# Performance work log

Measured on AMD Instinct MI355X. Metric: run time of the kernel, lower is better.

Reference implementation:

```python
import jax, jax.numpy as jnp
import numpy as np

D_MODEL = 1024
NUM_HEADS = 16
D_HEAD = D_MODEL // NUM_HEADS
MAX_SEQ_LEN = 4096
ROPE_THETA = 10000.0


def _rope_tables():
    freqs = 1.0 / (ROPE_THETA ** (jnp.arange(0, D_HEAD, 2, dtype=jnp.float32) / D_HEAD))
    pos = jnp.arange(MAX_SEQ_LEN, dtype=jnp.float32)
    ang = jnp.outer(pos, freqs)  # [max_seq, d_head/2]
    return jnp.cos(ang), jnp.sin(ang)


def apply_rope(x, token_positions, cos_tab, sin_tab):
    # x: [..., seq, d_head], token_positions: [batch, seq]
    cos = cos_tab[token_positions]  # [batch, seq, d_head/2]
    sin = sin_tab[token_positions]
    x_even = x[..., 0::2]
    x_odd = x[..., 1::2]
    e = x_even * cos - x_odd * sin
    o = x_even * sin + x_odd * cos
    # interleave back
    out = jnp.stack([e, o], axis=-1).reshape(x.shape)
    return out


def setup_inputs() -> dict:
    key = jax.random.key(0)
    k_x, k_q, k_k, k_v, k_o = jax.random.split(key, 5)
    B, S = 1, 4096
    x = jax.random.normal(k_x, (B, S, D_MODEL), dtype=jnp.float32)
    token_positions = jnp.broadcast_to(jnp.arange(S, dtype=jnp.int32)[None, :], (B, S))
    # trunc_normal init approximated by normal clipped to [-2, 2]
    def tn(k):
        return jnp.clip(jax.random.normal(k, (D_MODEL, D_MODEL), dtype=jnp.float32), -2.0, 2.0)
    return {
        "x": x,
        "token_positions": token_positions,
        "w_q": tn(k_q),
        "w_k": tn(k_k),
        "w_v": tn(k_v),
        "w_o": tn(k_o),
    }


def reference(x, token_positions, w_q, w_k, w_v, w_o):
    B, S, _ = x.shape
    cos_tab, sin_tab = _rope_tables()

    # Linear: y = x @ W^T  (weight is [out, in])
    Q = jnp.einsum('bsd,ed->bse', x, w_q)
    K = jnp.einsum('bsd,ed->bse', x, w_k)
    V = jnp.einsum('bsd,ed->bse', x, w_v)

    # [B, H, S, d_head]
    Q = Q.reshape(B, S, NUM_HEADS, D_HEAD).transpose(0, 2, 1, 3)
    K = K.reshape(B, S, NUM_HEADS, D_HEAD).transpose(0, 2, 1, 3)
    V = V.reshape(B, S, NUM_HEADS, D_HEAD).transpose(0, 2, 1, 3)

    # RoPE on Q, K (broadcast cos/sin over head dim)
    cos = cos_tab[token_positions][:, None]  # [B,1,S,d_head/2]
    sin = sin_tab[token_positions][:, None]
    def rope(t):
        e, o = t[..., 0::2], t[..., 1::2]
        return jnp.stack([e * cos - o * sin, e * sin + o * cos], axis=-1).reshape(t.shape)
    Q = rope(Q)
    K = rope(K)

    scale = 1.0 / jnp.sqrt(jnp.float32(D_HEAD))
    scores = jnp.einsum('bhqd,bhkd->bhqk', Q, K) * scale
    causal = jnp.tril(jnp.ones((S, S), dtype=bool))
    scores = jnp.where(causal, scores, -jnp.inf)
    probs = jax.nn.softmax(scores, axis=-1)
    attn = jnp.einsum('bhqk,bhkd->bhqd', probs, V)

    attn = attn.transpose(0, 2, 1, 3).reshape(B, S, D_MODEL)
    out = jnp.einsum('bsd,ed->bse', attn, w_o)
    return out
```

## Files before the change

kernel.cpp:

```cpp
#include <hip/hip_runtime.h>
#include <hip/hip_bf16.h>
#include <math.h>

#define S_LEN 4096
#define DMODEL 1024
#define NHEADS 16
#define DHEAD 64

typedef unsigned short u16;
typedef short bf16x8 __attribute__((ext_vector_type(8)));
typedef float f32x4 __attribute__((ext_vector_type(4)));
typedef u16 u16x4 __attribute__((ext_vector_type(4)));
typedef u16 u16x8 __attribute__((ext_vector_type(8)));
typedef unsigned uint4v __attribute__((ext_vector_type(4)));
typedef unsigned uint2v __attribute__((ext_vector_type(2)));

__device__ __forceinline__ u16 f2bf(float f) {
    unsigned u = __builtin_bit_cast(unsigned, f);
    u = (u + 0x7FFFu + ((u >> 16) & 1u)) >> 16;
    return (u16)u;
}
__device__ __forceinline__ float bf2f(u16 b) {
    return __builtin_bit_cast(float, ((unsigned)b) << 16);
}
__device__ __forceinline__ unsigned pack2bf(float lo, float hi) {
    __hip_bfloat162 c = __float22bfloat162_rn(make_float2(lo, hi));
    unsigned u;
    __builtin_memcpy(&u, &c, 4);
    return u;
}

__device__ __forceinline__ void gload16(const void* g, void* l) {
    __builtin_amdgcn_global_load_lds((const __attribute__((address_space(1))) void*)g,
                                     (__attribute__((address_space(3))) void*)l, 16, 0, 0);
}

__global__ void rope_table_kernel(float* __restrict__ cost, float* __restrict__ sint) {
    int tid = blockIdx.x * blockDim.x + threadIdx.x;
    int i = tid & 31;
    int pos = tid >> 5;
    double e = (double)(2 * i) / 64.0;
    float t32 = (float)pow(10000.0, e);
    float freq = 1.0f / t32;
    float ang = (float)pos * freq;
    cost[tid] = (float)cos((double)ang);
    sint[tid] = (float)sin((double)ang);
}

__global__ void split_kernel(const float* __restrict__ in, u16* __restrict__ hi,
                             u16* __restrict__ lo, int n4) {
    int i = blockIdx.x * blockDim.x + threadIdx.x;
    if (i >= n4) return;
    float4 v = ((const float4*)in)[i];
    float f[4] = {v.x, v.y, v.z, v.w};
    u16x4 h, l;
#pragma unroll
    for (int j = 0; j < 4; j++) {
        h[j] = f2bf(f[j]);
        l[j] = f2bf(f[j] - bf2f(h[j]));
    }
    ((u16x4*)hi)[i] = h;
    if (lo) ((u16x4*)lo)[i] = l;
}

__global__ __launch_bounds__(256) void gemm_qkv_kernel(
        const u16* __restrict__ xh, const u16* __restrict__ xl,
        const u16* __restrict__ wh3, const u16* __restrict__ wl3,
        const int* __restrict__ tp,
        const float* __restrict__ cost, const float* __restrict__ sint,
        u16* __restrict__ q2, u16* __restrict__ k2, u16* __restrict__ vtb) {
    __shared__ u16 sAH[2][128 * 32], sAL[2][128 * 32], sBH[2][128 * 32], sBL[2][128 * 32];
    const int z = blockIdx.z;
    const bool full = (z != 2);
    const u16* BH = wh3 + (size_t)z * 1048576;
    const u16* BL = wl3 + (size_t)z * 1048576;
    const int m0 = blockIdx.y * 128, n0 = blockIdx.x * 128;

    const int tid = threadIdx.x;
    const int lane = tid & 63, wid = tid >> 6;
    const int wr = wid >> 1, wc = wid & 1;
    const int l15 = lane & 15, lhi = lane >> 4;

    f32x4 acc[4][4];
#pragma unroll
    for (int i = 0; i < 4; i++)
#pragma unroll
        for (int j = 0; j < 4; j++) acc[i][j] = (f32x4){0.f, 0.f, 0.f, 0.f};

    auto stageT = [&](int kt, int b) {
#pragma unroll
        for (int i = 0; i < 2; i++) {
            const int rbase = wid * 32 + i * 16;
            const int row = rbase + (lane >> 2);
            const size_t aoff = (size_t)(m0 + row) * 1024 + kt + (lane & 3) * 8;
            const size_t boff = (size_t)(n0 + row) * 1024 + kt + (lane & 3) * 8;
            gload16(xh + aoff, sAH[b] + rbase * 32);
            gload16(BH + boff, sBH[b] + rbase * 32);
            if (full) {
                gload16(xl + aoff, sAL[b] + rbase * 32);
                gload16(BL + boff, sBL[b] + rbase * 32);
            }
        }
    };

    stageT(0, 0);
    __syncthreads();

    int buf = 0;
    for (int kt = 0; kt < 1024; kt += 32, buf ^= 1) {
        if (kt + 32 < 1024) stageT(kt + 32, buf ^ 1);
        bf16x8 ah[4], al[4], bh[4], bl[4];
#pragma unroll
        for (int m = 0; m < 4; m++) {
            int row = wr * 64 + m * 16 + l15;
            ah[m] = *(const bf16x8*)(sAH[buf] + row * 32 + 8 * lhi);
            if (full) al[m] = *(const bf16x8*)(sAL[buf] + row * 32 + 8 * lhi);
        }
#pragma unroll
        for (int n = 0; n < 4; n++) {
            int row = wc * 64 + n * 16 + l15;
            bh[n] = *(const bf16x8*)(sBH[buf] + row * 32 + 8 * lhi);
            if (full) bl[n] = *(const bf16x8*)(sBL[buf] + row * 32 + 8 * lhi);
        }
#pragma unroll
        for (int m = 0; m < 4; m++)
#pragma unroll
            for (int n = 0; n < 4; n++) {
                if (full) {
                    acc[m][n] = __builtin_amdgcn_mfma_f32_16x16x32_bf16(al[m], bh[n], acc[m][n], 0, 0, 0);
                    acc[m][n] = __builtin_amdgcn_mfma_f32_16x16x32_bf16(ah[m], bl[n], acc[m][n], 0, 0, 0);
                }
                acc[m][n] = __builtin_amdgcn_mfma_f32_16x16x32_bf16(ah[m], bh[n], acc[m][n], 0, 0, 0);
            }
        __syncthreads();
    }

    if (z == 2) {
#pragma unroll
        for (int m = 0; m < 4; m++)
#pragma unroll
            for (int n = 0; n < 4; n++)
#pragma unroll
                for (int j = 0; j < 4; j++) {
                    int srow = m0 + wr * 64 + m * 16 + lhi * 4 + j;
                    int eg = n0 + wc * 64 + n * 16 + l15;
                    vtb[(size_t)eg * S_LEN + srow] = f2bf(acc[m][n][j]);
                }
        return;
    }

    u16* outp = (z == 0) ? q2 : k2;
    const float qscale = (z == 0) ? 0.125f : 1.0f;
    const int head = (n0 + wc * 64) >> 6;
#pragma unroll
    for (int m = 0; m < 4; m++)
#pragma unroll
        for (int n = 0; n < 4; n++) {
            const int dh = n * 16 + l15;
            const int pairi = dh >> 1;
            const bool even = (dh & 1) == 0;
#pragma unroll
            for (int j = 0; j < 4; j++) {
                int srow = m0 + wr * 64 + m * 16 + lhi * 4 + j;
                float v = acc[m][n][j];
                float pv = __shfl_xor(v, 1);
                int pos = tp[srow];
                float cc = cost[(size_t)pos * 32 + pairi];
                float ss = sint[(size_t)pos * 32 + pairi];
                float e = even ? v : pv;
                float o = even ? pv : v;
                float res = (even ? (e * cc - o * ss) : (e * ss + o * cc)) * qscale;
                u16 hb = f2bf(res);
                u16 lb = f2bf(res - bf2f(hb));
                size_t base = ((size_t)head * S_LEN + srow) * 128 + dh;
                outp[base] = hb;
                outp[base + 64] = lb;
            }
        }
}

#define PLD32 36
__global__ __launch_bounds__(256) void attn_kernel(const u16* __restrict__ q2,
                                                   const u16* __restrict__ k2,
                                                   const u16* __restrict__ vtb,
                                                   u16* __restrict__ attnb) {
    const int h = blockIdx.y;
    const int p = blockIdx.x;
    const int wid = threadIdx.x >> 6;
    const int lane = threadIdx.x & 63;
    const int l15 = lane & 15, lhi = lane >> 4;

    const u16* Qh2 = q2 + (size_t)h * S_LEN * 128;
    const u16* Kh2 = k2 + (size_t)h * S_LEN * 128;
    const u16* Vh  = vtb + (size_t)h * 64 * S_LEN;

    __shared__ u16 sK[4][64 * 128];
    __shared__ u16 sV[4][64 * 64];
    __shared__ unsigned pls[4][32 * PLD32];
    unsigned* myP = pls[wid];

    const int tileA = 31 - p, tileB = p;
    const int eA = 2 * tileA + 2, eB = 2 * tileB + 2;
    const int etot = eA + eB;

    auto stage = [&](int t, int b) {
        const int k = (t < eA) ? t : (t - eA);
        const int k0 = k * 64;
#pragma unroll
        for (int i = 0; i < 4; i++) {
            const int rbase = wid * 16 + i * 4;
            const int row = rbase + (lane >> 4);
            const int cb = (lane & 15) * 16;
            const int csw = cb ^ ((row & 7) << 4);
            gload16(Kh2 + (size_t)(k0 + row) * 128 + (csw >> 1), &sK[b][rbase * 128]);
        }
#pragma unroll
        for (int i = 0; i < 2; i++) {
            const int rbase = wid * 16 + i * 8;
            const int row = rbase + (lane >> 3);
            const int cb = (lane & 7) * 16;
            const int csw = cb ^ ((row & 7) << 4);
            gload16(Vh + (size_t)row * S_LEN + k0 + (csw >> 1), &sV[b][rbase * 64]);
        }
    };

    bf16x8 qhf[2][2], qlf[2][2];
    f32x4 oT[2][4];
    float m_run[2], l_run[2];
    int q0 = 0, my_nkb = 0;

    auto initPass = [&](int tile) {
        q0 = tile * 128 + wid * 32;
        my_nkb = ((q0 + 31) >> 6) + 1;
#pragma unroll
        for (int g = 0; g < 2; g++)
#pragma unroll
            for (int ks = 0; ks < 2; ks++) {
                const u16* qp = Qh2 + (size_t)(q0 + g * 16 + l15) * 128 + ks * 32 + 8 * lhi;
                qhf[g][ks] = *(const bf16x8*)(qp);
                qlf[g][ks] = *(const bf16x8*)(qp + 64);
            }
#pragma unroll
        for (int g = 0; g < 2; g++) {
            m_run[g] = -1e30f;
            l_run[g] = 0.f;
#pragma unroll
            for (int m = 0; m < 4; m++) oT[g][m] = (f32x4){0.f, 0.f, 0.f, 0.f};
        }
    };

    auto writeOut = [&]() {
#pragma unroll
        for (int g = 0; g < 2; g++) {
            float lt = l_run[g];
            lt += __shfl_xor(lt, 16);
            lt += __shfl_xor(lt, 32);
            const float inv = 1.0f / lt;
            const int srow = q0 + g * 16 + l15;
#pragma unroll
            for (int m = 0; m < 4; m++)
#pragma unroll
                for (int j = 0; j < 4; j++)
                    attnb[(size_t)srow * 1024 + h * 64 + m * 16 + lhi * 4 + j] =
                        f2bf(oT[g][m][j] * inv);
        }
    };

    auto doStep = [&](int t, int b) {
        const int k = (t < eA) ? t : (t - eA);
        if (k >= my_nkb) return;
        const int k0 = k * 64;
        bf16x8 kh[4][2], kl[4][2], vfr[4][2];
#pragma unroll
        for (int m = 0; m < 4; m++) {
            const int r = m * 16 + l15;
            const int sw = (r & 7) << 4;
            const u16* kp = &sK[b][r * 128];
            const u16* vp = &sV[b][r * 64];
#pragma unroll
            for (int c = 0; c < 2; c++) {
                kh[m][c] = *(const bf16x8*)(kp + (((c * 64 + lhi * 16) ^ sw) >> 1));
                kl[m][c] = *(const bf16x8*)(kp + (((128 + c * 64 + lhi * 16) ^ sw) >> 1));
                vfr[m][c] = *(const bf16x8*)(vp + (((c * 64 + lhi * 16) ^ sw) >> 1));
            }
        }
        f32x4 sT[4][2];
#pragma unroll
        for (int m = 0; m < 4; m++)
#pragma unroll
            for (int g = 0; g < 2; g++) {
                f32x4 a = (f32x4){0.f, 0.f, 0.f, 0.f};
                a = __builtin_amdgcn_mfma_f32_16x16x32_bf16(kh[m][0], qlf[g][0], a, 0, 0, 0);
                a = __builtin_amdgcn_mfma_f32_16x16x32_bf16(kh[m][1], qlf[g][1], a, 0, 0, 0);
                a = __builtin_amdgcn_mfma_f32_16x16x32_bf16(kl[m][0], qhf[g][0], a, 0, 0, 0);
                a = __builtin_amdgcn_mfma_f32_16x16x32_bf16(kl[m][1], qhf[g][1], a, 0, 0, 0);
                a = __builtin_amdgcn_mfma_f32_16x16x32_bf16(kh[m][0], qhf[g][0], a, 0, 0, 0);
                a = __builtin_amdgcn_mfma_f32_16x16x32_bf16(kh[m][1], qhf[g][1], a, 0, 0, 0);
                sT[m][g] = a;
            }
        const bool last = (k == my_nkb - 1);
#pragma unroll
        for (int g = 0; g < 2; g++) {
            const int qg = q0 + g * 16 + l15;
            if (last) {
#pragma unroll
                for (int m = 0; m < 4; m++)
#pragma unroll
                    for (int j = 0; j < 4; j++) {
                        int kg = k0 + m * 16 + lhi * 4 + j;
                        if (kg > qg) sT[m][g][j] = -1e30f;
                    }
            }
            float t0 = fmaxf(fmaxf(sT[0][g][0], sT[0][g][1]), fmaxf(sT[0][g][2], sT[0][g][3]));
            float t1 = fmaxf(fmaxf(sT[1][g][0], sT[1][g][1]), fmaxf(sT[1][g][2], sT[1][g][3]));
            float t2 = fmaxf(fmaxf(sT[2][g][0], sT[2][g][1]), fmaxf(sT[2][g][2], sT[2][g][3]));
            float t3 = fmaxf(fmaxf(sT[3][g][0], sT[3][g][1]), fmaxf(sT[3][g][2], sT[3][g][3]));
            float lane_max = fmaxf(fmaxf(t0, t1), fmaxf(t2, t3));
            if (__any(lane_max > m_run[g] + 8.0f)) {
                float mx = fmaxf(m_run[g], lane_max);
                mx = fmaxf(mx, __shfl_xor(mx, 16));
                mx = fmaxf(mx, __shfl_xor(mx, 32));
                float alpha = __expf(m_run[g] - mx);
                l_run[g] *= alpha;
#pragma unroll
                for (int m = 0; m < 4; m++) {
                    oT[g][m][0] *= alpha; oT[g][m][1] *= alpha;
                    oT[g][m][2] *= alpha; oT[g][m][3] *= alpha;
                }
                m_run[g] = mx;
            }
            const float mr = m_run[g];
            float s0 = 0.f, s1 = 0.f, s2 = 0.f, s3 = 0.f;
#pragma unroll
            for (int m = 0; m < 4; m++) {
                float p0 = __expf(sT[m][g][0] - mr);
                float p1 = __expf(sT[m][g][1] - mr);
                float p2 = __expf(sT[m][g][2] - mr);
                float p3 = __expf(sT[m][g][3] - mr);
                sT[m][g][0] = p0; sT[m][g][1] = p1; sT[m][g][2] = p2; sT[m][g][3] = p3;
                s0 += p0; s1 += p1; s2 += p2; s3 += p3;
            }
            l_run[g] += (s0 + s1) + (s2 + s3);
#pragma unroll
            for (int m = 0; m < 4; m++) {
                uint2v pk;
                pk[0] = pack2bf(sT[m][g][0], sT[m][g][1]);
                pk[1] = pack2bf(sT[m][g][2], sT[m][g][3]);
                *(uint2v*)(myP + (g * 16 + l15) * PLD32 + m * 8 + lhi * 2) = pk;
            }
        }
        bf16x8 pf[2][2];
#pragma unroll
        for (int g = 0; g < 2; g++)
#pragma unroll
            for (int ks = 0; ks < 2; ks++) {
                uint4v pw = *(const uint4v*)(myP + (g * 16 + l15) * PLD32 + ks * 16 + 4 * lhi);
                pf[g][ks] = __builtin_bit_cast(bf16x8, pw);
            }
#pragma unroll
        for (int g = 0; g < 2; g++)
#pragma unroll
            for (int m = 0; m < 4; m++) {
                oT[g][m] = __builtin_amdgcn_mfma_f32_16x16x32_bf16(vfr[m][0], pf[g][0], oT[g][m], 0, 0, 0);
                oT[g][m] = __builtin_amdgcn_mfma_f32_16x16x32_bf16(vfr[m][1], pf[g][1], oT[g][m], 0, 0, 0);
            }
    };

    stage(0, 0);
    stage(1, 1);
    initPass(tileA);
    __syncthreads();

    for (int t = 0; t < etot; t += 2) {
        if (t + 2 < etot) stage(t + 2, (t + 2) & 3);
        if (t + 3 < etot) stage(t + 3, (t + 3) & 3);
        if (t == eA) { writeOut(); initPass(tileB); }
        doStep(t, t & 3);
        doStep(t + 1, (t + 1) & 3);
        __syncthreads();
    }
    writeOut();
}

__global__ __launch_bounds__(256) void gemm_out_kernel(const u16* __restrict__ attnb,
                                                       const u16* __restrict__ woh,
                                                       float* __restrict__ out) {
    __shared__ u16 sA[2][128 * 32];
    __shared__ u16 sB[2][128 * 32];
    const int m0 = blockIdx.y * 128, n0 = blockIdx.x * 128;
    const int tid = threadIdx.x;
    const int lane = tid & 63, wid = tid >> 6;
    const int wr = wid >> 1, wc = wid & 1;
    const int l15 = lane & 15, lhi = lane >> 4;

    f32x4 acc[4][4];
#pragma unroll
    for (int i = 0; i < 4; i++)
#pragma unroll
        for (int j = 0; j < 4; j++) acc[i][j] = (f32x4){0.f, 0.f, 0.f, 0.f};

    auto stageT = [&](int kt, int b) {
#pragma unroll
        for (int i = 0; i < 2; i++) {
            const int rbase = wid * 32 + i * 16;
            const int row = rbase + (lane >> 2);
            gload16(attnb + (size_t)(m0 + row) * 1024 + kt + (lane & 3) * 8, sA[b] + rbase * 32);
            gload16(woh + (size_t)(n0 + row) * 1024 + kt + (lane & 3) * 8, sB[b] + rbase * 32);
        }
    };

    stageT(0, 0);
    __syncthreads();

    int buf = 0;
    for (int kt = 0; kt < 1024; kt += 32, buf ^= 1) {
        if (kt + 32 < 1024) stageT(kt + 32, buf ^ 1);
        bf16x8 af[4], bfr[4];
#pragma unroll
        for (int m = 0; m < 4; m++) {
            int row = wr * 64 + m * 16 + l15;
            af[m] = *(const bf16x8*)(sA[buf] + row * 32 + 8 * lhi);
        }
#pragma unroll
        for (int n = 0; n < 4; n++) {
            int row = wc * 64 + n * 16 + l15;
            bfr[n] = *(const bf16x8*)(sB[buf] + row * 32 + 8 * lhi);
        }
#pragma unroll
        for (int m = 0; m < 4; m++)
#pragma unroll
            for (int n = 0; n < 4; n++)
                acc[m][n] = __builtin_amdgcn_mfma_f32_16x16x32_bf16(af[m], bfr[n], acc[m][n], 0, 0, 0);
        __syncthreads();
    }

#pragma unroll
    for (int m = 0; m < 4; m++)
#pragma unroll
        for (int n = 0; n < 4; n++)
#pragma unroll
            for (int j = 0; j < 4; j++) {
                int srow = m0 + wr * 64 + m * 16 + lhi * 4 + j;
                int eg = n0 + wc * 64 + n * 16 + l15;
                out[(size_t)srow * 1024 + eg] = acc[m][n][j];
            }
}

extern "C" void kernel_launch(void* const* d_in, const int* in_sizes, int n_in,
                              void* d_out, int out_size, void* d_ws, size_t ws_size,
                              hipStream_t stream) {
    const float* x = (const float*)d_in[0];
    const int* tp = (const int*)d_in[1];
    const float* wq = (const float*)d_in[2];
    const float* wk = (const float*)d_in[3];
    const float* wv = (const float*)d_in[4];
    const float* wo = (const float*)d_in[5];
    float* out = (float*)d_out;
    char* ws = (char*)d_ws;

    u16* Q2    = (u16*)(ws + 0);
    u16* K2    = (u16*)(ws + 16777216);
    u16* VTB   = (u16*)(ws + 33554432);
    u16* ATTNB = (u16*)(ws + 41943040);
    float* COST = (float*)(ws + 50331648);
    float* SINT = (float*)(ws + 50855936);
    u16* XH  = (u16*)(ws + 51380224);
    u16* XL  = (u16*)(ws + 59768832);
    u16* WH3 = (u16*)(ws + 68157440);
    u16* WL3 = (u16*)(ws + 74448896);
    u16* WOH = (u16*)(ws + 80740352);

    rope_table_kernel<<<512, 256, 0, stream>>>(COST, SINT);

    split_kernel<<<4096, 256, 0, stream>>>(x, XH, XL, 1048576);
    split_kernel<<<1024, 256, 0, stream>>>(wq, WH3,            WL3,            262144);
    split_kernel<<<1024, 256, 0, stream>>>(wk, WH3 + 1048576,  WL3 + 1048576,  262144);
    split_kernel<<<1024, 256, 0, stream>>>(wv, WH3 + 2097152,  WL3 + 2097152,  262144);
    split_kernel<<<1024, 256, 0, stream>>>(wo, WOH,            (u16*)nullptr,  262144);

    gemm_qkv_kernel<<<dim3(8, 32, 3), 256, 0, stream>>>(
        XH, XL, WH3, WL3, tp, COST, SINT, Q2, K2, VTB);

    attn_kernel<<<dim3(16, 16), 256, 0, stream>>>(Q2, K2, VTB, ATTNB);

    gemm_out_kernel<<<dim3(8, 32), 256, 0, stream>>>(ATTNB, WOH, out);
}
```

Before: 264.0 us.

## Split attention block across eight waves with sixteen query rows each

```diff
diff --git a/kernel.cpp b/kernel.cpp
--- a/kernel.cpp
+++ b/kernel.cpp
@@ -180,7 +180,7 @@
 }
 
 #define PLD32 36
-__global__ __launch_bounds__(256) void attn_kernel(const u16* __restrict__ q2,
+__global__ __launch_bounds__(512) void attn_kernel(const u16* __restrict__ q2,
                                                    const u16* __restrict__ k2,
                                                    const u16* __restrict__ vtb,
                                                    u16* __restrict__ attnb) {
@@ -196,7 +196,7 @@
 
     __shared__ u16 sK[4][64 * 128];
     __shared__ u16 sV[4][64 * 64];
-    __shared__ unsigned pls[4][32 * PLD32];
+    __shared__ unsigned pls[8][16 * PLD32];
     unsigned* myP = pls[wid];
 
     const int tileA = 31 - p, tileB = p;
@@ -207,16 +207,15 @@
         const int k = (t < eA) ? t : (t - eA);
         const int k0 = k * 64;
 #pragma unroll
-        for (int i = 0; i < 4; i++) {
-            const int rbase = wid * 16 + i * 4;
+        for (int i = 0; i < 2; i++) {
+            const int rbase = wid * 8 + i * 4;
             const int row = rbase + (lane >> 4);
             const int cb = (lane & 15) * 16;
             const int csw = cb ^ ((row & 7) << 4);
             gload16(Kh2 + (size_t)(k0 + row) * 128 + (csw >> 1), &sK[b][rbase * 128]);
         }
-#pragma unroll
-        for (int i = 0; i < 2; i++) {
-            const int rbase = wid * 16 + i * 8;
+        {
+            const int rbase = wid * 8;
             const int row = rbase + (lane >> 3);
             const int cb = (lane & 7) * 16;
             const int csw = cb ^ ((row & 7) << 4);
@@ -224,46 +223,38 @@
         }
     };
 
-    bf16x8 qhf[2][2], qlf[2][2];
-    f32x4 oT[2][4];
-    float m_run[2], l_run[2];
+    bf16x8 qhf[2], qlf[2];
+    f32x4 oT[4];
+    float m_run, l_run;
     int q0 = 0, my_nkb = 0;
 
     auto initPass = [&](int tile) {
-        q0 = tile * 128 + wid * 32;
-        my_nkb = ((q0 + 31) >> 6) + 1;
-#pragma unroll
-        for (int g = 0; g < 2; g++)
-#pragma unroll
-            for (int ks = 0; ks < 2; ks++) {
-                const u16* qp = Qh2 + (size_t)(q0 + g * 16 + l15) * 128 + ks * 32 + 8 * lhi;
-                qhf[g][ks] = *(const bf16x8*)(qp);
-                qlf[g][ks] = *(const bf16x8*)(qp + 64);
-            }
-#pragma unroll
-        for (int g = 0; g < 2; g++) {
-            m_run[g] = -1e30f;
-            l_run[g] = 0.f;
-#pragma unroll
-            for (int m = 0; m < 4; m++) oT[g][m] = (f32x4){0.f, 0.f, 0.f, 0.f};
-        }
+        q0 = tile * 128 + wid * 16;
+        my_nkb = ((q0 + 15) >> 6) + 1;
+#pragma unroll
+        for (int ks = 0; ks < 2; ks++) {
+            const u16* qp = Qh2 + (size_t)(q0 + l15) * 128 + ks * 32 + 8 * lhi;
+            qhf[ks] = *(const bf16x8*)(qp);
+            qlf[ks] = *(const bf16x8*)(qp + 64);
+        }
+        m_run = -1e30f;
+        l_run = 0.f;
+#pragma unroll
+        for (int m = 0; m < 4; m++) oT[m] = (f32x4){0.f, 0.f, 0.f, 0.f};
     };
 
     auto writeOut = [&]() {
-#pragma unroll
-        for (int g = 0; g < 2; g++) {
-            float lt = l_run[g];
-            lt += __shfl_xor(lt, 16);
-            lt += __shfl_xor(lt, 32);
-            const float inv = 1.0f / lt;
-            const int srow = q0 + g * 16 + l15;
-#pragma unroll
-            for (int m = 0; m < 4; m++)
-#pragma unroll
-                for (int j = 0; j < 4; j++)
-                    attnb[(size_t)srow * 1024 + h * 64 + m * 16 + lhi * 4 + j] =
-                        f2bf(oT[g][m][j] * inv);
-        }
+        float lt = l_run;
+        lt += __shfl_xor(lt, 16);
+        lt += __shfl_xor(lt, 32);
+        const float inv = 1.0f / lt;
+        const int srow = q0 + l15;
+#pragma unroll
+        for (int m = 0; m < 4; m++)
+#pragma unroll
+            for (int j = 0; j < 4; j++)
+                attnb[(size_t)srow * 1024 + h * 64 + m * 16 + lhi * 4 + j] =
+                    f2bf(oT[m][j] * inv);
     };
 
     auto doStep = [&](int t, int b) {
@@ -284,86 +275,77 @@
                 vfr[m][c] = *(const bf16x8*)(vp + (((c * 64 + lhi * 16) ^ sw) >> 1));
             }
         }
-        f32x4 sT[4][2];
-#pragma unroll
-        for (int m = 0; m < 4; m++)
-#pragma unroll
-            for (int g = 0; g < 2; g++) {
-                f32x4 a = (f32x4){0.f, 0.f, 0.f, 0.f};
-                a = __builtin_amdgcn_mfma_f32_16x16x32_bf16(kh[m][0], qlf[g][0], a, 0, 0, 0);
-                a = __builtin_amdgcn_mfma_f32_16x16x32_bf16(kh[m][1], qlf[g][1], a, 0, 0, 0);
-                a = __builtin_amdgcn_mfma_f32_16x16x32_bf16(kl[m][0], qhf[g][0], a, 0, 0, 0);
-                a = __builtin_amdgcn_mfma_f32_16x16x32_bf16(kl[m][1], qhf[g][1], a, 0, 0, 0);
-                a = __builtin_amdgcn_mfma_f32_16x16x32_bf16(kh[m][0], qhf[g][0], a, 0, 0, 0);
-                a = __builtin_amdgcn_mfma_f32_16x16x32_bf16(kh[m][1], qhf[g][1], a, 0, 0, 0);
-                sT[m][g] = a;
-            }
+        f32x4 sT[4];
+#pragma unroll
+        for (int m = 0; m < 4; m++) {
+            f32x4 a = (f32x4){0.f, 0.f, 0.f, 0.f};
+            a = __builtin_amdgcn_mfma_f32_16x16x32_bf16(kh[m][0], qlf[0], a, 0, 0, 0);
+            a = __builtin_amdgcn_mfma_f32_16x16x32_bf16(kh[m][1], qlf[1], a, 0, 0, 0);
+            a = __builtin_amdgcn_mfma_f32_16x16x32_bf16(kl[m][0], qhf[0], a, 0, 0, 0);
+            a = __builtin_amdgcn_mfma_f32_16x16x32_bf16(kl[m][1], qhf[1], a, 0, 0, 0);
+            a = __builtin_amdgcn_mfma_f32_16x16x32_bf16(kh[m][0], qhf[0], a, 0, 0, 0);
+            a = __builtin_amdgcn_mfma_f32_16x16x32_bf16(kh[m][1], qhf[1], a, 0, 0, 0);
+            sT[m] = a;
+        }
         const bool last = (k == my_nkb - 1);
-#pragma unroll
-        for (int g = 0; g < 2; g++) {
-            const int qg = q0 + g * 16 + l15;
-            if (last) {
-#pragma unroll
-                for (int m = 0; m < 4; m++)
-#pragma unroll
-                    for (int j = 0; j < 4; j++) {
-                        int kg = k0 + m * 16 + lhi * 4 + j;
-                        if (kg > qg) sT[m][g][j] = -1e30f;
-                    }
-            }
-            float t0 = fmaxf(fmaxf(sT[0][g][0], sT[0][g][1]), fmaxf(sT[0][g][2], sT[0][g][3]));
-            float t1 = fmaxf(fmaxf(sT[1][g][0], sT[1][g][1]), fmaxf(sT[1][g][2], sT[1][g][3]));
-            float t2 = fmaxf(fmaxf(sT[2][g][0], sT[2][g][1]), fmaxf(sT[2][g][2], sT[2][g][3]));
-            float t3 = fmaxf(fmaxf(sT[3][g][0], sT[3][g][1]), fmaxf(sT[3][g][2], sT[3][g][3]));
-            float lane_max = fmaxf(fmaxf(t0, t1), fmaxf(t2, t3));
-            if (__any(lane_max > m_run[g] + 8.0f)) {
-                float mx = fmaxf(m_run[g], lane_max);
-                mx = fmaxf(mx, __shfl_xor(mx, 16));
-                mx = fmaxf(mx, __shfl_xor(mx, 32));
-                float alpha = __expf(m_run[g] - mx);
-                l_run[g] *= alpha;
-#pragma unroll
-                for (int m = 0; m < 4; m++) {
-                    oT[g][m][0] *= alpha; oT[g][m][1] *= alpha;
-                    oT[g][m][2] *= alpha; oT[g][m][3] *= alpha;
+        const int qg = q0 + l15;
+        if (last) {
+#pragma unroll
+            for (int m = 0; m < 4; m++)
+#pragma unroll
+                for (int j = 0; j < 4; j++) {
+                    int kg = k0 + m * 16 + lhi * 4 + j;
+                    if (kg > qg) sT[m][j] = -1e30f;
                 }
-                m_run[g] = mx;
-            }
-            const float mr = m_run[g];
-            float s0 = 0.f, s1 = 0.f, s2 = 0.f, s3 = 0.f;
+        }
+        float t0 = fmaxf(fmaxf(sT[0][0], sT[0][1]), fmaxf(sT[0][2], sT[0][3]));
+        float t1 = fmaxf(fmaxf(sT[1][0], sT[1][1]), fmaxf(sT[1][2], sT[1][3]));
+        float t2 = fmaxf(fmaxf(sT[2][0], sT[2][1]), fmaxf(sT[2][2], sT[2][3]));
+        float t3 = fmaxf(fmaxf(sT[3][0], sT[3][1]), fmaxf(sT[3][2], sT[3][3]));
+        float lane_max = fmaxf(fmaxf(t0, t1), fmaxf(t2, t3));
+        if (__any(lane_max > m_run + 8.0f)) {
+            float mx = fmaxf(m_run, lane_max);
+            mx = fmaxf(mx, __shfl_xor(mx, 16));
+            mx = fmaxf(mx, __shfl_xor(mx, 32));
+            float alpha = __expf(m_run - mx);
+            l_run *= alpha;
 #pragma unroll
             for (int m = 0; m < 4; m++) {
-                float p0 = __expf(sT[m][g][0] - mr);
-                float p1 = __expf(sT[m][g][1] - mr);
-                float p2 = __expf(sT[m][g][2] - mr);
-                float p3 = __expf(sT[m][g][3] - mr);
-                sT[m][g][0] = p0; sT[m][g][1] = p1; sT[m][g][2] = p2; sT[m][g][3] = p3;
-                s0 += p0; s1 += p1; s2 += p2; s3 += p3;
-            }
-            l_run[g] += (s0 + s1) + (s2 + s3);
-#pragma unroll
-            for (int m = 0; m < 4; m++) {
-                uint2v pk;
-                pk[0] = pack2bf(sT[m][g][0], sT[m][g][1]);
-                pk[1] = pack2bf(sT[m][g][2], sT[m][g][3]);
-                *(uint2v*)(myP + (g * 16 + l15) * PLD32 + m * 8 + lhi * 2) = pk;
-            }
-        }
-        bf16x8 pf[2][2];
-#pragma unroll
-        for (int g = 0; g < 2; g++)
-#pragma unroll
-            for (int ks = 0; ks < 2; ks++) {
-                uint4v pw = *(const uint4v*)(myP + (g * 16 + l15) * PLD32 + ks * 16 + 4 * lhi);
-                pf[g][ks] = __builtin_bit_cast(bf16x8, pw);
-            }
-#pragma unroll
-        for (int g = 0; g < 2; g++)
-#pragma unroll
-            for (int m = 0; m < 4; m++) {
-                oT[g][m] = __builtin_amdgcn_mfma_f32_16x16x32_bf16(vfr[m][0], pf[g][0], oT[g][m], 0, 0, 0);
-                oT[g][m] = __builtin_amdgcn_mfma_f32_16x16x32_bf16(vfr[m][1], pf[g][1], oT[g][m], 0, 0, 0);
-            }
+                oT[m][0] *= alpha; oT[m][1] *= alpha;
+                oT[m][2] *= alpha; oT[m][3] *= alpha;
+            }
+            m_run = mx;
+        }
+        const float mr = m_run;
+        float s0 = 0.f, s1 = 0.f, s2 = 0.f, s3 = 0.f;
+#pragma unroll
+        for (int m = 0; m < 4; m++) {
+            float p0 = __expf(sT[m][0] - mr);
+            float p1 = __expf(sT[m][1] - mr);
+            float p2 = __expf(sT[m][2] - mr);
+            float p3 = __expf(sT[m][3] - mr);
+            sT[m][0] = p0; sT[m][1] = p1; sT[m][2] = p2; sT[m][3] = p3;
+            s0 += p0; s1 += p1; s2 += p2; s3 += p3;
+        }
+        l_run += (s0 + s1) + (s2 + s3);
+#pragma unroll
+        for (int m = 0; m < 4; m++) {
+            uint2v pk;
+            pk[0] = pack2bf(sT[m][0], sT[m][1]);
+            pk[1] = pack2bf(sT[m][2], sT[m][3]);
+            *(uint2v*)(myP + l15 * PLD32 + m * 8 + lhi * 2) = pk;
+        }
+        bf16x8 pf[2];
+#pragma unroll
+        for (int ks = 0; ks < 2; ks++) {
+            uint4v pw = *(const uint4v*)(myP + l15 * PLD32 + ks * 16 + 4 * lhi);
+            pf[ks] = __builtin_bit_cast(bf16x8, pw);
+        }
+#pragma unroll
+        for (int m = 0; m < 4; m++) {
+            oT[m] = __builtin_amdgcn_mfma_f32_16x16x32_bf16(vfr[m][0], pf[0], oT[m], 0, 0, 0);
+            oT[m] = __builtin_amdgcn_mfma_f32_16x16x32_bf16(vfr[m][1], pf[1], oT[m], 0, 0, 0);
+        }
     };
 
     stage(0, 0);
@@ -481,7 +463,7 @@
     gemm_qkv_kernel<<<dim3(8, 32, 3), 256, 0, stream>>>(
         XH, XL, WH3, WL3, tp, COST, SINT, Q2, K2, VTB);
 
-    attn_kernel<<<dim3(16, 16), 256, 0, stream>>>(Q2, K2, VTB, ATTNB);
+    attn_kernel<<<dim3(16, 16), 512, 0, stream>>>(Q2, K2, VTB, ATTNB);
 
     gemm_out_kernel<<<dim3(8, 32), 256, 0, stream>>>(ATTNB, WOH, out);
 }
```

Result: faster. 230.4 us (-12.7%).
